# Kernel optimization log

Measured on AMD Instinct MI355X. Metric: run time of the kernel, lower is better.

Reference implementation:

```python
import jax, jax.numpy as jnp
import numpy as np

N = 100_000   # nodes
E = 1_600_000 # edges (avg degree 16)
F = 128       # in_features
H = 128       # hidden_size


def setup_inputs() -> dict:
    key = jax.random.key(0)
    ks = jax.random.split(key, 9)
    glorot = lambda k, fi, fo: jax.random.uniform(
        k, (fi, fo), jnp.float32, -np.sqrt(6.0 / (fi + fo)), np.sqrt(6.0 / (fi + fo)))
    return {
        "feat": jax.random.uniform(ks[0], (N, F), jnp.float32, 1e-3, 1.0),
        "edge_index": jax.random.randint(ks[1], (2, E), 0, N, jnp.int32),
        "edge_weight": jax.random.uniform(ks[2], (E,), jnp.float32, 0.1, 1.0),
        "W0": glorot(ks[3], F, H), "b0": jnp.zeros((H,), jnp.float32),
        "W1": glorot(ks[4], H, H), "b1": jnp.zeros((H,), jnp.float32),
        "W2": glorot(ks[5], H, 1), "b2": jnp.zeros((1,), jnp.float32),
    }


def _gcn_norm(edge_index, edge_weight, num_nodes):
    # GCNConv default: add self-loops (weight 1), symmetric normalization.
    row, col = edge_index[0], edge_index[1]
    loop = jnp.arange(num_nodes, dtype=edge_index.dtype)
    row = jnp.concatenate([row, loop])
    col = jnp.concatenate([col, loop])
    w = jnp.concatenate([edge_weight, jnp.ones((num_nodes,), edge_weight.dtype)])
    deg = jax.ops.segment_sum(w, col, num_segments=num_nodes)  # in-degree over targets
    dinv = jnp.where(deg > 0, jax.lax.rsqrt(deg), 0.0)
    norm = dinv[row] * w * dinv[col]
    return row, col, norm


def _gcn_conv(x, W, b, row, col, norm, num_nodes):
    xp = x @ W                                   # [N, out]
    msg = xp[row] * norm[:, None]                # gather + weight  [E', out]
    out = jax.ops.segment_sum(msg, col, num_segments=num_nodes)  # scatter-add
    return out + b


def reference(feat, edge_index, edge_weight, W0, b0, W1, b1, W2, b2):
    num_nodes = feat.shape[0]
    feat = feat / feat.sum(axis=1, keepdims=True)
    row, col, norm = _gcn_norm(edge_index, edge_weight, num_nodes)
    h = jax.nn.relu(_gcn_conv(feat, W0, b0, row, col, norm, num_nodes))
    h = jax.nn.relu(_gcn_conv(h, W1, b1, row, col, norm, num_nodes))
    out = _gcn_conv(h, W2, b2, row, col, norm, num_nodes)  # [N, 1]
    return out
```

## Files before the change

kernel.cpp:

```cpp
#include <hip/hip_runtime.h>

#define NF 128
typedef unsigned long long ull;
typedef unsigned int uint;


__device__ __forceinline__ float bflo(uint u) { return __uint_as_float(u << 16); }
__device__ __forceinline__ float bfhi(uint u) { return __uint_as_float(u & 0xffff0000u); }
__device__ __forceinline__ uint pack_bf16(float a, float b) {
  uint ua = __float_as_uint(a), ub = __float_as_uint(b);
  ua = (ua + 0x7fffu + ((ua >> 16) & 1u)) >> 16;
  ub = (ub + 0x7fffu + ((ub >> 16) & 1u)) & 0xffff0000u;
  return ua | ub;
}

__device__ __forceinline__ uint pack_edge(uint row, float nrm) {
  uint q = __float2uint_rn(nrm * 32768.0f);
  q = q > 32767u ? 32767u : q;
  return (q << 17) | row;
}


__global__ __launch_bounds__(256) void k_pre1(const int* __restrict__ col,
                                              const float* __restrict__ w,
                                              ull* __restrict__ packed,
                                              uint* __restrict__ rank, int ne, int gE,
                                              const float* __restrict__ feat,
                                              float* __restrict__ invs, int n) {
  if (blockIdx.x < (uint)gE) {
    int e = blockIdx.x * 256 + threadIdx.x;
    if (e >= ne) return;
    int c = col[e];
    unsigned fix = (unsigned)__float2uint_rn(w[e] * 16777216.0f);
    ull old = atomicAdd(&packed[c], ((ull)fix << 32) | 1ull);
    rank[e] = (uint)(old & 0xffffffffu);
  } else {
    int gid = (blockIdx.x - gE) * 256 + threadIdx.x;
    int wave = gid >> 6, lane = gid & 63;
    if (wave >= n) return;
    float2 v = ((const float2*)(feat + (size_t)wave * NF))[lane];
    float s = v.x + v.y;
#pragma unroll
    for (int off = 1; off < 64; off <<= 1) s += __shfl_xor(s, off, 64);
    if (lane == 0) invs[wave] = 1.0f / s;
  }
}


__global__ __launch_bounds__(256) void k_scan_local(const ull* __restrict__ packed,
                                                    int* __restrict__ excl,
                                                    int* __restrict__ bsum,
                                                    float* __restrict__ dinv, int n) {
  __shared__ int sd[256];
  int tid = threadIdx.x;
  int idx = blockIdx.x * 1024 + tid * 4;
  int4 v = {0, 0, 0, 0};
  const float k24 = 1.0f / 16777216.0f;
  if (idx + 4 <= n) {
    ull p0 = packed[idx], p1 = packed[idx + 1], p2 = packed[idx + 2], p3 = packed[idx + 3];
    v.x = (int)(uint)p0; v.y = (int)(uint)p1; v.z = (int)(uint)p2; v.w = (int)(uint)p3;
    float4 dv;
    dv.x = rsqrtf((float)(uint)(p0 >> 32) * k24 + 1.0f);
    dv.y = rsqrtf((float)(uint)(p1 >> 32) * k24 + 1.0f);
    dv.z = rsqrtf((float)(uint)(p2 >> 32) * k24 + 1.0f);
    dv.w = rsqrtf((float)(uint)(p3 >> 32) * k24 + 1.0f);
    *(float4*)&dinv[idx] = dv;
  } else {
    for (int k = 0; k < 4; ++k) {
      if (idx + k < n) {
        ull p = packed[idx + k];
        ((int*)&v)[k] = (int)(uint)p;
        dinv[idx + k] = rsqrtf((float)(uint)(p >> 32) * k24 + 1.0f);
      }
    }
  }
  int tsum = v.x + v.y + v.z + v.w;
  sd[tid] = tsum;
  __syncthreads();
  for (int off = 1; off < 256; off <<= 1) {
    int t = (tid >= off) ? sd[tid - off] : 0;
    __syncthreads();
    sd[tid] += t;
    __syncthreads();
  }
  int texcl = sd[tid] - tsum;
  if (tid == 255) bsum[blockIdx.x] = sd[255];
  int4 w;
  w.x = texcl; w.y = texcl + v.x; w.z = texcl + v.x + v.y; w.w = texcl + v.x + v.y + v.z;
  if (idx + 4 <= n) {
    *(int4*)&excl[idx] = w;
  } else {
    if (idx < n)     excl[idx] = w.x;
    if (idx + 1 < n) excl[idx + 1] = w.y;
    if (idx + 2 < n) excl[idx + 2] = w.z;
    if (idx + 3 < n) excl[idx + 3] = w.w;
  }
}

__global__ __launch_bounds__(256) void k_scan_sums(const int* __restrict__ bsum,
                                                   int* __restrict__ bexcl,
                                                   int* __restrict__ rowptr_end, int nb) {
  __shared__ int sd[256];
  int tid = threadIdx.x;
  int v = (tid < nb) ? bsum[tid] : 0;
  sd[tid] = v;
  __syncthreads();
  for (int off = 1; off < 256; off <<= 1) {
    int t = (tid >= off) ? sd[tid - off] : 0;
    __syncthreads();
    sd[tid] += t;
    __syncthreads();
  }
  if (tid < nb) bexcl[tid] = sd[tid] - v;
  if (tid == 255) rowptr_end[0] = sd[255];
}

__global__ __launch_bounds__(256) void k_scan_add(int* __restrict__ rowptr,
                                                  const int* __restrict__ bexcl, int n) {
  int i = blockIdx.x * 256 + threadIdx.x;
  if (i >= n) return;
  rowptr[i] += bexcl[i >> 10];
}


__device__ __forceinline__ void gemm_body(const float* __restrict__ X,
                                          const float* __restrict__ W,
                                          uint* __restrict__ Yb, int n,
                                          const float* __restrict__ scale,
                                          int bid, int tid,
                                          float* Ws, float* Xs) {
  for (int i = tid * 4; i < 128 * 128; i += 256 * 4)
    *(float4*)&Ws[i] = *(const float4*)&W[i];

  int r0 = bid * 64;
  int tcol = tid & 15, trow = tid >> 4;
  float acc[4][8] = {};

  for (int kc = 0; kc < 128; kc += 32) {
    __syncthreads();
    {
      int rr = tid >> 2;
      int cc = (tid & 3) * 8;
      int grow = r0 + rr;
      if (grow >= n) grow = n - 1;
      float sc = scale ? scale[grow] : 1.0f;
      const float* src = X + (size_t)grow * NF + kc + cc;
      float4 a = *(const float4*)src;
      float4 b = *(const float4*)(src + 4);
      a.x *= sc; a.y *= sc; a.z *= sc; a.w *= sc;
      b.x *= sc; b.y *= sc; b.z *= sc; b.w *= sc;
      *(float4*)&Xs[rr * 36 + cc] = a;
      *(float4*)&Xs[rr * 36 + cc + 4] = b;
    }
    __syncthreads();
#pragma unroll
    for (int k4 = 0; k4 < 32; k4 += 4) {
      float4 xv[4];
#pragma unroll
      for (int i = 0; i < 4; i++)
        xv[i] = *(const float4*)&Xs[(trow * 4 + i) * 36 + k4];
#pragma unroll
      for (int kk = 0; kk < 4; kk++) {
        float4 w0 = *(const float4*)&Ws[(kc + k4 + kk) * 128 + tcol * 4];
        float4 w1 = *(const float4*)&Ws[(kc + k4 + kk) * 128 + 64 + tcol * 4];
#pragma unroll
        for (int i = 0; i < 4; i++) {
          float xx = ((const float*)&xv[i])[kk];
          acc[i][0] = fmaf(xx, w0.x, acc[i][0]);
          acc[i][1] = fmaf(xx, w0.y, acc[i][1]);
          acc[i][2] = fmaf(xx, w0.z, acc[i][2]);
          acc[i][3] = fmaf(xx, w0.w, acc[i][3]);
          acc[i][4] = fmaf(xx, w1.x, acc[i][4]);
          acc[i][5] = fmaf(xx, w1.y, acc[i][5]);
          acc[i][6] = fmaf(xx, w1.z, acc[i][6]);
          acc[i][7] = fmaf(xx, w1.w, acc[i][7]);
        }
      }
    }
  }
#pragma unroll
  for (int i = 0; i < 4; i++) {
    int gr = r0 + trow * 4 + i;
    if (gr < n) {
      uint2 p0 = {pack_bf16(acc[i][0], acc[i][1]), pack_bf16(acc[i][2], acc[i][3])};
      uint2 p1 = {pack_bf16(acc[i][4], acc[i][5]), pack_bf16(acc[i][6], acc[i][7])};
      *(uint2*)&Yb[(size_t)gr * 64 + tcol * 2] = p0;
      *(uint2*)&Yb[(size_t)gr * 64 + 32 + tcol * 2] = p1;
    }
  }
}


__global__ __launch_bounds__(256, 2) void k_sc_gemm(const int* __restrict__ row,
                                                    const int* __restrict__ col,
                                                    const float* __restrict__ w,
                                                    const float* __restrict__ dinv,
                                                    const int* __restrict__ rowptr,
                                                    const uint* __restrict__ rank,
                                                    uint* __restrict__ sEdge, int ne, int gE,
                                                    const float* __restrict__ X,
                                                    const float* __restrict__ W0,
                                                    const float* __restrict__ invs,
                                                    uint* __restrict__ Yb, int n) {
  __shared__ float Ws[128 * 128];
  __shared__ float Xs[64 * 36];
  if (blockIdx.x < (uint)gE) {
    int e = blockIdx.x * 256 + threadIdx.x;
    if (e >= ne) return;
    int r = row[e], c = col[e];
    int pos = rowptr[c] + (int)rank[e];
    float nrm = dinv[r] * w[e];
    sEdge[pos] = pack_edge((uint)r, nrm);
    return;
  }
  gemm_body(X, W0, Yb, n, invs, blockIdx.x - gE, threadIdx.x, Ws, Xs);
}

__global__ __launch_bounds__(256, 2) void k_gemm128(const float* __restrict__ X,
                                                    const float* __restrict__ W,
                                                    uint* __restrict__ Yb, int n) {
  __shared__ float Ws[128 * 128];
  __shared__ float Xs[64 * 36];
  gemm_body(X, W, Yb, n, nullptr, blockIdx.x, threadIdx.x, Ws, Xs);
}


#define AGG_PROLOGUE \
  int gid = blockIdx.x * 256 + threadIdx.x; \
  int i = gid >> 4; \
  int lane = gid & 15; \
  if (i >= n) return; \
  float di = dinv[i]; \
  uint4 xv = ((const uint4*)XPb)[(size_t)i * 16 + lane]; \
  int s = rowptr[i], e = rowptr[i + 1]; \
  float acc[8] = {0.f, 0.f, 0.f, 0.f, 0.f, 0.f, 0.f, 0.f}; \
  int j = s;

#define GATHER(en, g) \
  uint4 g = ((const uint4*)XPb)[(size_t)((en) & 0x1FFFFu) * 16 + lane];
#define ACCUM(en, g) { \
  float nr = (float)((en) >> 17) * (1.0f / 32768.0f); \
  acc[0] = fmaf(bflo(g.x), nr, acc[0]); acc[1] = fmaf(bfhi(g.x), nr, acc[1]); \
  acc[2] = fmaf(bflo(g.y), nr, acc[2]); acc[3] = fmaf(bfhi(g.y), nr, acc[3]); \
  acc[4] = fmaf(bflo(g.z), nr, acc[4]); acc[5] = fmaf(bfhi(g.z), nr, acc[5]); \
  acc[6] = fmaf(bflo(g.w), nr, acc[6]); acc[7] = fmaf(bfhi(g.w), nr, acc[7]); }

#define AGG_EDGE_LOOP \
  for (; j + 8 <= e; j += 8) { \
    uint e0 = sEdge[j],     e1 = sEdge[j + 1], e2 = sEdge[j + 2], e3 = sEdge[j + 3]; \
    uint e4 = sEdge[j + 4], e5 = sEdge[j + 5], e6 = sEdge[j + 6], e7 = sEdge[j + 7]; \
    GATHER(e0, g0) GATHER(e1, g1) GATHER(e2, g2) GATHER(e3, g3) \
    GATHER(e4, g4) GATHER(e5, g5) GATHER(e6, g6) GATHER(e7, g7) \
    ACCUM(e0, g0) ACCUM(e1, g1) ACCUM(e2, g2) ACCUM(e3, g3) \
    ACCUM(e4, g4) ACCUM(e5, g5) ACCUM(e6, g6) ACCUM(e7, g7) \
  } \
  if (j + 4 <= e) { \
    uint e0 = sEdge[j], e1 = sEdge[j + 1], e2 = sEdge[j + 2], e3 = sEdge[j + 3]; \
    GATHER(e0, g0) GATHER(e1, g1) GATHER(e2, g2) GATHER(e3, g3) \
    ACCUM(e0, g0) ACCUM(e1, g1) ACCUM(e2, g2) ACCUM(e3, g3) \
    j += 4; \
  } \
  for (; j < e; ++j) { \
    uint e0 = sEdge[j]; \
    GATHER(e0, g0) \
    ACCUM(e0, g0) \
  }

#define AGG_FINISH(o0, o1, bias) \
  float sn = di * di; \
  float4 o0, o1; \
  { \
    float4 bA = ((const float4*)bias)[lane * 2]; \
    float4 bB = ((const float4*)bias)[lane * 2 + 1]; \
    o0.x = fmaf(acc[0], di, fmaf(bflo(xv.x), sn, bA.x)); \
    o0.y = fmaf(acc[1], di, fmaf(bfhi(xv.x), sn, bA.y)); \
    o0.z = fmaf(acc[2], di, fmaf(bflo(xv.y), sn, bA.z)); \
    o0.w = fmaf(acc[3], di, fmaf(bfhi(xv.y), sn, bA.w)); \
    o1.x = fmaf(acc[4], di, fmaf(bflo(xv.z), sn, bB.x)); \
    o1.y = fmaf(acc[5], di, fmaf(bfhi(xv.z), sn, bB.y)); \
    o1.z = fmaf(acc[6], di, fmaf(bflo(xv.w), sn, bB.z)); \
    o1.w = fmaf(acc[7], di, fmaf(bfhi(xv.w), sn, bB.w)); \
    o0.x = fmaxf(o0.x, 0.f); o0.y = fmaxf(o0.y, 0.f); \
    o0.z = fmaxf(o0.z, 0.f); o0.w = fmaxf(o0.w, 0.f); \
    o1.x = fmaxf(o1.x, 0.f); o1.y = fmaxf(o1.y, 0.f); \
    o1.z = fmaxf(o1.z, 0.f); o1.w = fmaxf(o1.w, 0.f); \
  }

__global__ __launch_bounds__(256) void k_agg128b(const uint* __restrict__ XPb,
                                                 const int* __restrict__ rowptr,
                                                 const uint* __restrict__ sEdge,
                                                 const float* __restrict__ dinv,
                                                 const float* __restrict__ bias,
                                                 float* __restrict__ Y, int n) {
  AGG_PROLOGUE
  AGG_EDGE_LOOP
  AGG_FINISH(o0, o1, bias)
  ((float4*)(Y + (size_t)i * NF))[lane * 2] = o0;
  ((float4*)(Y + (size_t)i * NF))[lane * 2 + 1] = o1;
}

__global__ __launch_bounds__(256) void k_agg_gemv(const uint* __restrict__ XPb,
                                                  const int* __restrict__ rowptr,
                                                  const uint* __restrict__ sEdge,
                                                  const float* __restrict__ dinv,
                                                  const float* __restrict__ bias,
                                                  const float* __restrict__ w2,
                                                  float* __restrict__ xp2, int n) {
  AGG_PROLOGUE
  AGG_EDGE_LOOP
  AGG_FINISH(o0, o1, bias)
  float4 wA = ((const float4*)w2)[lane * 2];
  float4 wB = ((const float4*)w2)[lane * 2 + 1];
  float sdot = o0.x * wA.x + o0.y * wA.y + o0.z * wA.z + o0.w * wA.w +
               o1.x * wB.x + o1.y * wB.y + o1.z * wB.z + o1.w * wB.w;
  sdot += __shfl_xor(sdot, 1, 64);
  sdot += __shfl_xor(sdot, 2, 64);
  sdot += __shfl_xor(sdot, 4, 64);
  sdot += __shfl_xor(sdot, 8, 64);
  if (lane == 0) xp2[i] = sdot;
}


__global__ __launch_bounds__(256) void k_agg1(const float* __restrict__ xp2,
                                              const int* __restrict__ rowptr,
                                              const uint* __restrict__ sEdge,
                                              const float* __restrict__ dinv,
                                              const float* __restrict__ b2,
                                              float* __restrict__ out, int n) {
  int i = blockIdx.x * 256 + threadIdx.x;
  if (i >= n) return;
  float di = dinv[i];
  float accE = 0.0f;
  int s = rowptr[i], e = rowptr[i + 1];
  int j = s;
  for (; j + 4 <= e; j += 4) {
    uint e0 = sEdge[j], e1 = sEdge[j + 1], e2 = sEdge[j + 2], e3 = sEdge[j + 3];
    float v0 = xp2[e0 & 0x1FFFFu], v1 = xp2[e1 & 0x1FFFFu];
    float v2 = xp2[e2 & 0x1FFFFu], v3 = xp2[e3 & 0x1FFFFu];
    accE = fmaf(v0, (float)(e0 >> 17) * (1.0f / 32768.0f), accE);
    accE = fmaf(v1, (float)(e1 >> 17) * (1.0f / 32768.0f), accE);
    accE = fmaf(v2, (float)(e2 >> 17) * (1.0f / 32768.0f), accE);
    accE = fmaf(v3, (float)(e3 >> 17) * (1.0f / 32768.0f), accE);
  }
  for (; j < e; ++j) {
    uint e0 = sEdge[j];
    accE = fmaf(xp2[e0 & 0x1FFFFu], (float)(e0 >> 17) * (1.0f / 32768.0f), accE);
  }
  out[i] = fmaf(accE, di, fmaf(xp2[i], di * di, b2[0]));
}


extern "C" void kernel_launch(void* const* d_in, const int* in_sizes, int n_in,
                              void* d_out, int out_size, void* d_ws, size_t ws_size,
                              hipStream_t stream) {
  const float* feat = (const float*)d_in[0];
  const int* ei = (const int*)d_in[1];
  const float* ew = (const float*)d_in[2];
  const float* W0 = (const float*)d_in[3];
  const float* b0 = (const float*)d_in[4];
  const float* W1 = (const float*)d_in[5];
  const float* b1 = (const float*)d_in[6];
  const float* W2 = (const float*)d_in[7];
  const float* b2 = (const float*)d_in[8];
  float* out = (float*)d_out;

  const int N_ = in_sizes[0] / NF;
  const int E_ = in_sizes[2];
  const int* row = ei;
  const int* col = ei + E_;

  char* ws = (char*)d_ws;
  size_t off = 0;
  auto alloc = [&](size_t bytes) -> void* {
    void* p = ws + off;
    off = (off + bytes + 255) & ~(size_t)255;
    return p;
  };
  float* bufA  = (float*)alloc((size_t)N_ * NF * 4);
  uint*  bufBb = (uint*) alloc((size_t)N_ * NF * 2);
  ull*   packed= (ull*)  alloc((size_t)N_ * 8);
  float* dinv  = (float*)alloc((size_t)N_ * 4);
  float* invs  = (float*)alloc((size_t)N_ * 4);
  int*   rowptr= (int*)  alloc(((size_t)N_ + 1) * 4);
  int*   bsum  = (int*)  alloc(256 * 4);
  int*   bexcl = (int*)  alloc(256 * 4);
  uint*  rank  = (uint*) alloc((size_t)E_ * 4);
  uint*  sEdge = (uint*) alloc((size_t)E_ * 4);
  float* xp2   = (float*)alloc((size_t)N_ * 4);

  const int nThreads = 256;
  const int gN   = (N_ + nThreads - 1) / nThreads;
  const int gE   = (E_ + nThreads - 1) / nThreads;
  const int gWav = (N_ + 3) / 4;
  const int gAgg = (N_ + 15) / 16;
  const int gGemm = (N_ + 63) / 64;
  const int nScanBlocks = (N_ + 1023) / 1024;

  hipMemsetAsync(packed, 0, (size_t)N_ * 8, stream);
  k_pre1<<<gE + gWav, nThreads, 0, stream>>>(col, ew, packed, rank, E_, gE,
                                             feat, invs, N_);
  k_scan_local<<<nScanBlocks, nThreads, 0, stream>>>(packed, rowptr, bsum, dinv, N_);
  k_scan_sums<<<1, nThreads, 0, stream>>>(bsum, bexcl, rowptr + N_, nScanBlocks);
  k_scan_add<<<gN, nThreads, 0, stream>>>(rowptr, bexcl, N_);
  k_sc_gemm<<<gE + gGemm, nThreads, 0, stream>>>(row, col, ew, dinv, rowptr, rank,
                                                 sEdge, E_, gE,
                                                 feat, W0, invs, bufBb, N_);
  k_agg128b<<<gAgg, nThreads, 0, stream>>>(bufBb, rowptr, sEdge, dinv, b0, bufA, N_);
  k_gemm128<<<gGemm, nThreads, 0, stream>>>(bufA, W1, bufBb, N_);
  k_agg_gemv<<<gAgg, nThreads, 0, stream>>>(bufBb, rowptr, sEdge, dinv, b1, W2, xp2, N_);
  k_agg1<<<gN, nThreads, 0, stream>>>(xp2, rowptr, sEdge, dinv, b2, out, N_);
}
```

Baseline: 483.2 us.

## Replace global-atomic CSR build with two-level bucketed counting sort

Builds the target-sorted edge list with a two-pass radix-style sort instead of global 64-bit atomics per edge. Edges are tiled, coarse-bucketed by column high bits using LDS histograms and scans, then each bucket is finely sorted in LDS, which also yields rowptr and dinv. A separate pass folds dinv[row] into the quantized edge weights. This removes heavy contention on global atomics and the random scatter, but adds several kernel launches and an 8-byte intermediate pass, and the GEMM is no longer overlapped with the edge scatter.

```diff
diff --git a/kernel.cpp b/kernel.cpp
--- a/kernel.cpp
+++ b/kernel.cpp
@@ -1,6 +1,9 @@
 #include <hip/hip_runtime.h>
 
 #define NF 128
+#define TILE_E 8192
+#define BKT_SHIFT 9
+#define BKT_COLS 512
 typedef unsigned long long ull;
 typedef unsigned int uint;
 
@@ -21,118 +24,181 @@
 }
 
 
-__global__ __launch_bounds__(256) void k_pre1(const int* __restrict__ col,
-                                              const float* __restrict__ w,
-                                              ull* __restrict__ packed,
-                                              uint* __restrict__ rank, int ne, int gE,
-                                              const float* __restrict__ feat,
-                                              float* __restrict__ invs, int n) {
-  if (blockIdx.x < (uint)gE) {
-    int e = blockIdx.x * 256 + threadIdx.x;
-    if (e >= ne) return;
-    int c = col[e];
-    unsigned fix = (unsigned)__float2uint_rn(w[e] * 16777216.0f);
-    ull old = atomicAdd(&packed[c], ((ull)fix << 32) | 1ull);
-    rank[e] = (uint)(old & 0xffffffffu);
+__global__ __launch_bounds__(256) void k_hist_rowsum(const int* __restrict__ col,
+                                                     uint* __restrict__ hist,
+                                                     int ne, int nT,
+                                                     const float* __restrict__ feat,
+                                                     float* __restrict__ invs, int n) {
+  if ((int)blockIdx.x < nT) {
+    __shared__ uint lh[256];
+    int tid = threadIdx.x;
+    lh[tid] = 0;
+    __syncthreads();
+    int base = blockIdx.x * TILE_E;
+    int lim = min(ne - base, TILE_E);
+    for (int k = tid; k < lim; k += 256) {
+      int c = col[base + k];
+      atomicAdd(&lh[c >> BKT_SHIFT], 1u);
+    }
+    __syncthreads();
+    hist[(size_t)tid * nT + blockIdx.x] = lh[tid];
   } else {
-    int gid = (blockIdx.x - gE) * 256 + threadIdx.x;
+    int gid = ((int)blockIdx.x - nT) * 256 + threadIdx.x;
     int wave = gid >> 6, lane = gid & 63;
     if (wave >= n) return;
     float2 v = ((const float2*)(feat + (size_t)wave * NF))[lane];
     float s = v.x + v.y;
-#pragma unroll
     for (int off = 1; off < 64; off <<= 1) s += __shfl_xor(s, off, 64);
     if (lane == 0) invs[wave] = 1.0f / s;
   }
 }
 
 
-__global__ __launch_bounds__(256) void k_scan_local(const ull* __restrict__ packed,
-                                                    int* __restrict__ excl,
-                                                    int* __restrict__ bsum,
-                                                    float* __restrict__ dinv, int n) {
+__global__ __launch_bounds__(256) void k_scan_tiles(const uint* __restrict__ hist,
+                                                    uint* __restrict__ tbb,
+                                                    uint* __restrict__ btot, int nT) {
+  __shared__ uint sd[256];
+  int b = blockIdx.x, tid = threadIdx.x;
+  uint v = (tid < nT) ? hist[(size_t)b * nT + tid] : 0u;
+  sd[tid] = v;
+  __syncthreads();
+  for (int off = 1; off < 256; off <<= 1) {
+    uint t = (tid >= off) ? sd[tid - off] : 0u;
+    __syncthreads();
+    sd[tid] += t;
+    __syncthreads();
+  }
+  if (tid < nT) tbb[(size_t)b * nT + tid] = sd[tid] - v;
+  if (tid == 255) btot[b] = sd[255];
+}
+
+
+__global__ __launch_bounds__(256) void k_scan_buckets(const uint* __restrict__ btot,
+                                                      uint* __restrict__ bbase,
+                                                      int* __restrict__ rowptrN,
+                                                      int nB, int ne) {
+  __shared__ uint sd[256];
+  int tid = threadIdx.x;
+  uint v = (tid < nB) ? btot[tid] : 0u;
+  sd[tid] = v;
+  __syncthreads();
+  for (int off = 1; off < 256; off <<= 1) {
+    uint t = (tid >= off) ? sd[tid - off] : 0u;
+    __syncthreads();
+    sd[tid] += t;
+    __syncthreads();
+  }
+  if (tid < nB) bbase[tid] = sd[tid] - v;
+  if (tid == nB - 1) bbase[nB] = sd[tid];
+  if (tid == 0) rowptrN[0] = ne;
+}
+
+
+__global__ __launch_bounds__(256) void k_coarse(const int* __restrict__ row,
+                                                const int* __restrict__ col,
+                                                const float* __restrict__ w,
+                                                const uint* __restrict__ tbb,
+                                                const uint* __restrict__ bbase,
+                                                uint2* __restrict__ bstore,
+                                                int ne, int nT, int nB) {
+  __shared__ uint cur[256];
+  int t = blockIdx.x, tid = threadIdx.x;
+  cur[tid] = (tid < nB) ? (bbase[tid] + tbb[(size_t)tid * nT + t]) : 0u;
+  __syncthreads();
+  int base = t * TILE_E;
+  int lim = min(ne - base, TILE_E);
+  for (int k = tid; k < lim; k += 256) {
+    int e = base + k;
+    int c = col[e];
+    uint pos = atomicAdd(&cur[c >> BKT_SHIFT], 1u);
+    bstore[pos] = make_uint2(((uint)(c & (BKT_COLS - 1)) << 17) | (uint)row[e],
+                             __float_as_uint(w[e]));
+  }
+}
+
+
+__global__ __launch_bounds__(256) void k_fine(const uint2* __restrict__ bstore,
+                                              const uint* __restrict__ bbase,
+                                              int* __restrict__ rowptr,
+                                              float* __restrict__ dinv,
+                                              uint* __restrict__ sEdge, int n) {
+  __shared__ int hcnt[BKT_COLS];
+  __shared__ int hws[BKT_COLS];
+  __shared__ int cur[BKT_COLS];
   __shared__ int sd[256];
-  int tid = threadIdx.x;
-  int idx = blockIdx.x * 1024 + tid * 4;
-  int4 v = {0, 0, 0, 0};
-  const float k24 = 1.0f / 16777216.0f;
-  if (idx + 4 <= n) {
-    ull p0 = packed[idx], p1 = packed[idx + 1], p2 = packed[idx + 2], p3 = packed[idx + 3];
-    v.x = (int)(uint)p0; v.y = (int)(uint)p1; v.z = (int)(uint)p2; v.w = (int)(uint)p3;
-    float4 dv;
-    dv.x = rsqrtf((float)(uint)(p0 >> 32) * k24 + 1.0f);
-    dv.y = rsqrtf((float)(uint)(p1 >> 32) * k24 + 1.0f);
-    dv.z = rsqrtf((float)(uint)(p2 >> 32) * k24 + 1.0f);
-    dv.w = rsqrtf((float)(uint)(p3 >> 32) * k24 + 1.0f);
-    *(float4*)&dinv[idx] = dv;
-  } else {
-    for (int k = 0; k < 4; ++k) {
-      if (idx + k < n) {
-        ull p = packed[idx + k];
-        ((int*)&v)[k] = (int)(uint)p;
-        dinv[idx + k] = rsqrtf((float)(uint)(p >> 32) * k24 + 1.0f);
-      }
-    }
-  }
-  int tsum = v.x + v.y + v.z + v.w;
-  sd[tid] = tsum;
+  int b = blockIdx.x, tid = threadIdx.x;
+  int start = (int)bbase[b], end = (int)bbase[b + 1];
+  hcnt[tid] = 0; hcnt[tid + 256] = 0;
+  hws[tid] = 0;  hws[tid + 256] = 0;
+  __syncthreads();
+  for (int i = start + tid; i < end; i += 256) {
+    uint2 v = bstore[i];
+    int cl = (int)(v.x >> 17);
+    atomicAdd(&hcnt[cl], 1);
+    int wf = (int)__float2uint_rn(__uint_as_float(v.y) * 16777216.0f);
+    atomicAdd(&hws[cl], wf);
+  }
+  __syncthreads();
+  int a0 = hcnt[2 * tid], a1 = hcnt[2 * tid + 1];
+  int ps = a0 + a1;
+  sd[tid] = ps;
   __syncthreads();
   for (int off = 1; off < 256; off <<= 1) {
-    int t = (tid >= off) ? sd[tid - off] : 0;
-    __syncthreads();
-    sd[tid] += t;
-    __syncthreads();
-  }
-  int texcl = sd[tid] - tsum;
-  if (tid == 255) bsum[blockIdx.x] = sd[255];
-  int4 w;
-  w.x = texcl; w.y = texcl + v.x; w.z = texcl + v.x + v.y; w.w = texcl + v.x + v.y + v.z;
-  if (idx + 4 <= n) {
-    *(int4*)&excl[idx] = w;
-  } else {
-    if (idx < n)     excl[idx] = w.x;
-    if (idx + 1 < n) excl[idx + 1] = w.y;
-    if (idx + 2 < n) excl[idx + 2] = w.z;
-    if (idx + 3 < n) excl[idx + 3] = w.w;
-  }
-}
-
-__global__ __launch_bounds__(256) void k_scan_sums(const int* __restrict__ bsum,
-                                                   int* __restrict__ bexcl,
-                                                   int* __restrict__ rowptr_end, int nb) {
-  __shared__ int sd[256];
-  int tid = threadIdx.x;
-  int v = (tid < nb) ? bsum[tid] : 0;
-  sd[tid] = v;
-  __syncthreads();
-  for (int off = 1; off < 256; off <<= 1) {
-    int t = (tid >= off) ? sd[tid - off] : 0;
-    __syncthreads();
-    sd[tid] += t;
-    __syncthreads();
-  }
-  if (tid < nb) bexcl[tid] = sd[tid] - v;
-  if (tid == 255) rowptr_end[0] = sd[255];
-}
-
-__global__ __launch_bounds__(256) void k_scan_add(int* __restrict__ rowptr,
-                                                  const int* __restrict__ bexcl, int n) {
+    int tv = (tid >= off) ? sd[tid - off] : 0;
+    __syncthreads();
+    sd[tid] += tv;
+    __syncthreads();
+  }
+  int pexcl = sd[tid] - ps;
+  cur[2 * tid] = pexcl;
+  cur[2 * tid + 1] = pexcl + a0;
+  {
+    const float k24 = 1.0f / 16777216.0f;
+    int c0 = b * BKT_COLS + 2 * tid;
+    if (c0 < n) {
+      rowptr[c0] = start + pexcl;
+      dinv[c0] = rsqrtf((float)hws[2 * tid] * k24 + 1.0f);
+    }
+    if (c0 + 1 < n) {
+      rowptr[c0 + 1] = start + pexcl + a0;
+      dinv[c0 + 1] = rsqrtf((float)hws[2 * tid + 1] * k24 + 1.0f);
+    }
+  }
+  __syncthreads();
+  for (int i = start + tid; i < end; i += 256) {
+    uint2 v = bstore[i];
+    int cl = (int)(v.x >> 17);
+    int pos = start + atomicAdd(&cur[cl], 1);
+    float wv = __uint_as_float(v.y);
+    uint wq = __float2uint_rn(wv * 32768.0f);
+    wq = wq > 32767u ? 32767u : wq;
+    sEdge[pos] = (wq << 17) | (v.x & 0x1FFFFu);
+  }
+}
+
+
+__global__ __launch_bounds__(256) void k_fix(uint* __restrict__ sEdge,
+                                             const float* __restrict__ dinv, int ne) {
   int i = blockIdx.x * 256 + threadIdx.x;
-  if (i >= n) return;
-  rowptr[i] += bexcl[i >> 10];
-}
-
-
-__device__ __forceinline__ void gemm_body(const float* __restrict__ X,
-                                          const float* __restrict__ W,
-                                          uint* __restrict__ Yb, int n,
-                                          const float* __restrict__ scale,
-                                          int bid, int tid,
-                                          float* Ws, float* Xs) {
+  if (i >= ne) return;
+  uint en = sEdge[i];
+  uint r = en & 0x1FFFFu;
+  float wv = (float)(en >> 17) * (1.0f / 32768.0f);
+  sEdge[i] = pack_edge(r, dinv[r] * wv);
+}
+
+
+__global__ __launch_bounds__(256, 2) void k_gemm128(const float* __restrict__ X,
+                                                    const float* __restrict__ W,
+                                                    uint* __restrict__ Yb, int n,
+                                                    const float* __restrict__ scale) {
+  __shared__ float Ws[128 * 128];
+  __shared__ float Xs[64 * 36];
+  const int tid = threadIdx.x;
   for (int i = tid * 4; i < 128 * 128; i += 256 * 4)
     *(float4*)&Ws[i] = *(const float4*)&W[i];
 
-  int r0 = bid * 64;
+  int r0 = blockIdx.x * 64;
   int tcol = tid & 15, trow = tid >> 4;
   float acc[4][8] = {};
 
@@ -191,40 +257,6 @@
 }
 
 
-__global__ __launch_bounds__(256, 2) void k_sc_gemm(const int* __restrict__ row,
-                                                    const int* __restrict__ col,
-                                                    const float* __restrict__ w,
-                                                    const float* __restrict__ dinv,
-                                                    const int* __restrict__ rowptr,
-                                                    const uint* __restrict__ rank,
-                                                    uint* __restrict__ sEdge, int ne, int gE,
-                                                    const float* __restrict__ X,
-                                                    const float* __restrict__ W0,
-                                                    const float* __restrict__ invs,
-                                                    uint* __restrict__ Yb, int n) {
-  __shared__ float Ws[128 * 128];
-  __shared__ float Xs[64 * 36];
-  if (blockIdx.x < (uint)gE) {
-    int e = blockIdx.x * 256 + threadIdx.x;
-    if (e >= ne) return;
-    int r = row[e], c = col[e];
-    int pos = rowptr[c] + (int)rank[e];
-    float nrm = dinv[r] * w[e];
-    sEdge[pos] = pack_edge((uint)r, nrm);
-    return;
-  }
-  gemm_body(X, W0, Yb, n, invs, blockIdx.x - gE, threadIdx.x, Ws, Xs);
-}
-
-__global__ __launch_bounds__(256, 2) void k_gemm128(const float* __restrict__ X,
-                                                    const float* __restrict__ W,
-                                                    uint* __restrict__ Yb, int n) {
-  __shared__ float Ws[128 * 128];
-  __shared__ float Xs[64 * 36];
-  gemm_body(X, W, Yb, n, nullptr, blockIdx.x, threadIdx.x, Ws, Xs);
-}
-
-
 #define AGG_PROLOGUE \
   int gid = blockIdx.x * 256 + threadIdx.x; \
   int i = gid >> 4; \
@@ -376,16 +408,20 @@
     off = (off + bytes + 255) & ~(size_t)255;
     return p;
   };
+  const int nT = (E_ + TILE_E - 1) / TILE_E;
+  const int nB = (N_ + BKT_COLS - 1) / BKT_COLS;
+
   float* bufA  = (float*)alloc((size_t)N_ * NF * 4);
   uint*  bufBb = (uint*) alloc((size_t)N_ * NF * 2);
-  ull*   packed= (ull*)  alloc((size_t)N_ * 8);
+  uint2* bstore= (uint2*)alloc((size_t)E_ * 8);
+  uint*  sEdge = (uint*) alloc((size_t)E_ * 4);
+  uint*  hist  = (uint*) alloc((size_t)256 * nT * 4);
+  uint*  tbb   = (uint*) alloc((size_t)256 * nT * 4);
+  uint*  btot  = (uint*) alloc(256 * 4);
+  uint*  bbase = (uint*) alloc(257 * 4);
   float* dinv  = (float*)alloc((size_t)N_ * 4);
   float* invs  = (float*)alloc((size_t)N_ * 4);
   int*   rowptr= (int*)  alloc(((size_t)N_ + 1) * 4);
-  int*   bsum  = (int*)  alloc(256 * 4);
-  int*   bexcl = (int*)  alloc(256 * 4);
-  uint*  rank  = (uint*) alloc((size_t)E_ * 4);
-  uint*  sEdge = (uint*) alloc((size_t)E_ * 4);
   float* xp2   = (float*)alloc((size_t)N_ * 4);
 
   const int nThreads = 256;
@@ -394,19 +430,17 @@
   const int gWav = (N_ + 3) / 4;
   const int gAgg = (N_ + 15) / 16;
   const int gGemm = (N_ + 63) / 64;
-  const int nScanBlocks = (N_ + 1023) / 1024;
-
-  hipMemsetAsync(packed, 0, (size_t)N_ * 8, stream);
-  k_pre1<<<gE + gWav, nThreads, 0, stream>>>(col, ew, packed, rank, E_, gE,
-                                             feat, invs, N_);
-  k_scan_local<<<nScanBlocks, nThreads, 0, stream>>>(packed, rowptr, bsum, dinv, N_);
-  k_scan_sums<<<1, nThreads, 0, stream>>>(bsum, bexcl, rowptr + N_, nScanBlocks);
-  k_scan_add<<<gN, nThreads, 0, stream>>>(rowptr, bexcl, N_);
-  k_sc_gemm<<<gE + gGemm, nThreads, 0, stream>>>(row, col, ew, dinv, rowptr, rank,
-                                                 sEdge, E_, gE,
-                                                 feat, W0, invs, bufBb, N_);
+
+  k_hist_rowsum<<<nT + gWav, nThreads, 0, stream>>>(col, hist, E_, nT, feat, invs, N_);
+  k_scan_tiles<<<nB, nThreads, 0, stream>>>(hist, tbb, btot, nT);
+  k_scan_buckets<<<1, nThreads, 0, stream>>>(btot, bbase, rowptr + N_, nB, E_);
+  k_coarse<<<nT, nThreads, 0, stream>>>(row, col, ew, tbb, bbase, bstore, E_, nT, nB);
+  k_fine<<<nB, nThreads, 0, stream>>>(bstore, bbase, rowptr, dinv, sEdge, N_);
+  k_fix<<<gE, nThreads, 0, stream>>>(sEdge, dinv, E_);
+
+  k_gemm128<<<gGemm, nThreads, 0, stream>>>(feat, W0, bufBb, N_, invs);
   k_agg128b<<<gAgg, nThreads, 0, stream>>>(bufBb, rowptr, sEdge, dinv, b0, bufA, N_);
-  k_gemm128<<<gGemm, nThreads, 0, stream>>>(bufA, W1, bufBb, N_);
+  k_gemm128<<<gGemm, nThreads, 0, stream>>>(bufA, W1, bufBb, N_, nullptr);
   k_agg_gemv<<<gAgg, nThreads, 0, stream>>>(bufBb, rowptr, sEdge, dinv, b1, W2, xp2, N_);
   k_agg1<<<gN, nThreads, 0, stream>>>(xp2, rowptr, sEdge, dinv, b2, out, N_);
 }
```

Result: faster. 427.4 us (-11.5%).
